# Performance work log

Hardware: AMD Instinct MI355X
Metric: run time of the kernel (lower is better)

Reference implementation:

```python
import jax, jax.numpy as jnp
import numpy as np

B, S, D, H = 2, 2048, 1024, 16
DH = D // H

def setup_inputs() -> dict:
    key = jax.random.key(0)
    ks = jax.random.split(key, 6)
    scale = 0.02
    return {
        "x":  jax.random.normal(ks[0], (B, S, D), jnp.float32),
        "Wq": jax.random.normal(ks[1], (D, D), jnp.float32) * scale,
        "Wk": jax.random.normal(ks[2], (D, D), jnp.float32) * scale,
        "Wv": jax.random.normal(ks[3], (D, D), jnp.float32) * scale,
        "Wo": jax.random.normal(ks[4], (D, D), jnp.float32) * scale,
        "bo": jnp.zeros((D,), jnp.float32),
    }

def reference(x, Wq, Wk, Wv, Wo, bo):
    b, s, d = x.shape
    h, dh = H, DH
    # projections -> [b, h, s, dh]
    def split_heads(t):
        return t.reshape(b, s, h, dh).transpose(0, 2, 1, 3)
    q = split_heads(x @ Wq)
    k = split_heads(x @ Wk)
    v = split_heads(x @ Wv)
    # scaled causal attention
    scores = jnp.einsum('bhqd,bhkd->bhqk', q, k) / jnp.sqrt(jnp.float32(dh))
    causal = jnp.tril(jnp.ones((s, s), bool))
    scores = jnp.where(causal[None, None], scores, -jnp.inf)
    attn = jax.nn.softmax(scores, axis=-1)
    # dropout p=0.0 -> identity
    ctx = jnp.einsum('bhqk,bhkd->bhqd', attn, v)
    ctx = ctx.transpose(0, 2, 1, 3).reshape(b, s, d)
    return ctx @ Wo + bo
```

## Files before the change

### kernel.cpp

```cpp
#include <hip/hip_runtime.h>


typedef _Float16 f16;
typedef _Float16 f16x8 __attribute__((ext_vector_type(8)));
typedef _Float16 f16x4 __attribute__((ext_vector_type(4)));
typedef float    f32x4 __attribute__((ext_vector_type(4)));

__device__ __forceinline__ void gload16(const void* g, void* l) {
  __builtin_amdgcn_global_load_lds(
      (const __attribute__((address_space(1))) void*)g,
      (__attribute__((address_space(3))) void*)l, 16, 0, 0);
}

__global__ void cvt_x(const float* __restrict__ x, f16* __restrict__ xb) {
  int idx = blockIdx.x * 256 + threadIdx.x;
  float4 v = ((const float4*)x)[idx];
  f16x4 o = { (f16)v.x, (f16)v.y, (f16)v.z, (f16)v.w };
  ((f16x4*)xb)[idx] = o;
}

__global__ void cvt_w(const float* __restrict__ W0, const float* __restrict__ W1,
                      const float* __restrict__ W2, const float* __restrict__ W3,
                      f16* __restrict__ T0, f16* __restrict__ T1,
                      f16* __restrict__ T2, f16* __restrict__ T3) {
  const float* W = blockIdx.z == 0 ? W0 : blockIdx.z == 1 ? W1 : blockIdx.z == 2 ? W2 : W3;
  f16*        Tt = blockIdx.z == 0 ? T0 : blockIdx.z == 1 ? T1 : blockIdx.z == 2 ? T2 : T3;
  __shared__ f16 tile[64][65];
  int tid = threadIdx.x;
  int k0 = blockIdx.y * 64, n0 = blockIdx.x * 64;
  int rr = tid >> 4, cc = (tid & 15) * 4;
#pragma unroll
  for (int p = 0; p < 4; ++p) {
    int r = rr + p * 16;
    float4 v = *(const float4*)(W + (size_t)(k0 + r) * 1024 + n0 + cc);
    tile[r][cc + 0] = (f16)v.x; tile[r][cc + 1] = (f16)v.y;
    tile[r][cc + 2] = (f16)v.z; tile[r][cc + 3] = (f16)v.w;
  }
  __syncthreads();
#pragma unroll
  for (int p = 0; p < 4; ++p) {
    int r = rr + p * 16;
    f16x4 v;
#pragma unroll
    for (int j = 0; j < 4; ++j) v[j] = tile[cc + j][r];
    *(f16x4*)(Tt + (size_t)(n0 + r) * 1024 + k0 + cc) = v;
  }
}

template <int MODE>
__global__ __launch_bounds__(256, 2)
void gemm_k(const f16* __restrict__ A, const f16* __restrict__ Bt,
            f16* __restrict__ oQ, f16* __restrict__ oK, f16* __restrict__ oV,
            float* __restrict__ oO, const float* __restrict__ bias) {
  constexpr int Kd = 1024;
  __shared__ f16 smem[2 * 128 * 64];
  f16* sA = smem;
  f16* sB = smem + 128 * 64;
  const int tid = threadIdx.x;
  const int lane = tid & 63, wid = tid >> 6;
  const int wr = wid >> 1, wc = wid & 1;
  const int bm = blockIdx.y * 128, bn = blockIdx.x * 128;

  f32x4 acc[4][4] = {};

  for (int k0 = 0; k0 < Kd; k0 += 64) {
#pragma unroll
    for (int p = 0; p < 4; ++p) {
      int c = p * 256 + tid;
      int row = c >> 3;
      int gc = (c & 7) ^ (row & 7);
      gload16(A + (size_t)(bm + row) * Kd + k0 + gc * 8, sA + c * 8);
      gload16(Bt + (size_t)(bn + row) * Kd + k0 + gc * 8, sB + c * 8);
    }
    __syncthreads();
#pragma unroll
    for (int ks = 0; ks < 2; ++ks) {
      f16x8 af[4], bf[4];
#pragma unroll
      for (int m = 0; m < 4; ++m) {
        int row = wr * 64 + m * 16 + (lane & 15);
        int j = (ks * 4 + (lane >> 4)) ^ (row & 7);
        af[m] = *(const f16x8*)((const char*)sA + row * 128 + j * 16);
      }
#pragma unroll
      for (int n = 0; n < 4; ++n) {
        int row = wc * 64 + n * 16 + (lane & 15);
        int j = (ks * 4 + (lane >> 4)) ^ (row & 7);
        bf[n] = *(const f16x8*)((const char*)sB + row * 128 + j * 16);
      }
#pragma unroll
      for (int m = 0; m < 4; ++m)
#pragma unroll
        for (int n = 0; n < 4; ++n)
          acc[m][n] = __builtin_amdgcn_mfma_f32_16x16x32_f16(af[m], bf[n], acc[m][n], 0, 0, 0);
    }
    __syncthreads();
  }

  if constexpr (MODE == 2) {
#pragma unroll
    for (int m = 0; m < 4; ++m) {
      int rbase = bm + wr * 64 + m * 16 + ((lane >> 4) << 2);
#pragma unroll
      for (int n = 0; n < 4; ++n) {
        int ncol = bn + wc * 64 + n * 16 + (lane & 15);
        float bv = bias[ncol];
#pragma unroll
        for (int i = 0; i < 4; ++i)
          oO[(size_t)(rbase + i) * 1024 + ncol] = acc[m][n][i] + bv;
      }
    }
  } else {
    const int seg = bn >> 10;
    if (seg < 2) {
      f16* dst = seg == 0 ? oQ : oK;
#pragma unroll
      for (int m = 0; m < 4; ++m) {
        int rbase = bm + wr * 64 + m * 16 + ((lane >> 4) << 2);
#pragma unroll
        for (int n = 0; n < 4; ++n) {
          int ncol = (bn & 1023) + wc * 64 + n * 16 + (lane & 15);
          int h = ncol >> 6, dh = ncol & 63;
#pragma unroll
          for (int i = 0; i < 4; ++i) {
            int rr = rbase + i;
            int b = rr >> 11, s = rr & 2047;
            dst[(((size_t)(b * 16 + h) * 2048 + s) << 6) + dh] = (f16)acc[m][n][i];
          }
        }
      }
    } else {
      f16* T64 = smem;
      int b = bm >> 11, sbase = bm & 2047;
      int bnl = bn & 1023;
#pragma unroll
      for (int p = 0; p < 2; ++p) {
        if (wr == p) {
#pragma unroll
          for (int m = 0; m < 4; ++m)
#pragma unroll
            for (int n = 0; n < 4; ++n)
#pragma unroll
              for (int i = 0; i < 4; ++i) {
                int rl = m * 16 + ((lane >> 4) << 2) + i;
                int col = wc * 64 + n * 16 + (lane & 15);
                T64[rl * 132 + col] = (f16)acc[m][n][i];
              }
        }
        __syncthreads();
#pragma unroll
        for (int it = 0; it < 4; ++it) {
          int oc = it * 256 + tid;
          int ocol = oc >> 3;
          int och = oc & 7;
          f16x8 v;
#pragma unroll
          for (int j = 0; j < 8; ++j) v[j] = T64[(och * 8 + j) * 132 + ocol];
          int ncol = bnl + ocol;
          int h = ncol >> 6, dh = ncol & 63;
          *(f16x8*)(oV + ((size_t)((b * 16 + h) * 64 + dh) << 11) + sbase + p * 64 + och * 8) = v;
        }
        __syncthreads();
      }
    }
  }
}

__global__ __launch_bounds__(256, 2)
void attn_k(const f16* __restrict__ Q, const f16* __restrict__ Kg,
            const f16* __restrict__ Vt, f16* __restrict__ ctx) {
  __shared__ f16 sK[64 * 64];
  __shared__ f16 sV[64 * 64];
  __shared__ f16 sP[4][16 * 64];
  const int tid = threadIdx.x, lane = tid & 63, wid = tid >> 6;
  const int bh = blockIdx.y;
  const int b = bh >> 4, h = bh & 15;
  const f16* Qb = Q + ((size_t)bh << 17);
  const f16* Kb = Kg + ((size_t)bh << 17);
  const f16* Vb = Vt + ((size_t)bh << 17);
  const float SC = 0.1803368801f;

  for (int half = 0; half < 2; ++half) {
    const int qt = half == 0 ? blockIdx.x : 31 - blockIdx.x;
    const int qbase = qt * 64 + wid * 16;
    const int qg = qbase + (lane & 15);
    const int qmax_w = qbase + 15;

    const int qrow_a = qbase + (lane & 15);
    f16x8 qf[2];
    qf[0] = *(const f16x8*)(Qb + (size_t)qrow_a * 64 + ((lane >> 4) << 3));
    qf[1] = *(const f16x8*)(Qb + (size_t)qrow_a * 64 + 32 + ((lane >> 4) << 3));

    f32x4 acc[4] = {};
    float m_run = -INFINITY, l_run = 0.f;

    for (int kt = 0; kt <= qt; ++kt) {
#pragma unroll
      for (int p = 0; p < 2; ++p) {
        int c = p * 256 + tid;
        int row = c >> 3;
        int gc = (c & 7) ^ (row & 7);
        gload16(Kb + (size_t)(kt * 64 + row) * 64 + gc * 8, sK + c * 8);
        gload16(Vb + (size_t)row * 2048 + kt * 64 + gc * 8, sV + c * 8);
      }
      __syncthreads();

      f32x4 sf[4];
#pragma unroll
      for (int kc = 0; kc < 4; ++kc) {
        if (kt * 64 + kc * 16 <= qmax_w) {
          f32x4 z = {};
#pragma unroll
          for (int ks = 0; ks < 2; ++ks) {
            int row = kc * 16 + (lane & 15);
            int j = (ks * 4 + (lane >> 4)) ^ (row & 7);
            f16x8 kf = *(const f16x8*)((const char*)sK + row * 128 + j * 16);
            z = __builtin_amdgcn_mfma_f32_16x16x32_f16(kf, qf[ks], z, 0, 0, 0);
          }
          sf[kc] = z;
        } else {
          sf[kc] = (f32x4){-1e30f, -1e30f, -1e30f, -1e30f};
        }
      }
#pragma unroll
      for (int kc = 0; kc < 4; ++kc) {
        if (kt * 64 + kc * 16 + 15 > qbase) {
#pragma unroll
          for (int i = 0; i < 4; ++i) {
            int kg = kt * 64 + kc * 16 + ((lane >> 4) << 2) + i;
            sf[kc][i] = (kg <= qg) ? sf[kc][i] * SC : -1e30f;
          }
        } else {
#pragma unroll
          for (int i = 0; i < 4; ++i) sf[kc][i] *= SC;
        }
      }
      float v01 = fmaxf(fmaxf(sf[0][0], sf[0][1]), fmaxf(sf[0][2], sf[0][3]));
      float v23 = fmaxf(fmaxf(sf[1][0], sf[1][1]), fmaxf(sf[1][2], sf[1][3]));
      float v45 = fmaxf(fmaxf(sf[2][0], sf[2][1]), fmaxf(sf[2][2], sf[2][3]));
      float v67 = fmaxf(fmaxf(sf[3][0], sf[3][1]), fmaxf(sf[3][2], sf[3][3]));
      float v = fmaxf(fmaxf(v01, v23), fmaxf(v45, v67));
      v = fmaxf(v, __shfl_xor(v, 16));
      v = fmaxf(v, __shfl_xor(v, 32));
      float mn = fmaxf(m_run, v);
      float scl = __builtin_amdgcn_exp2f(m_run - mn);
      m_run = mn;
      float ls = 0.f;
#pragma unroll
      for (int kc = 0; kc < 4; ++kc)
#pragma unroll
        for (int i = 0; i < 4; ++i) {
          float p = __builtin_amdgcn_exp2f(sf[kc][i] - mn);
          sf[kc][i] = p;
          ls += p;
        }
      ls += __shfl_xor(ls, 16);
      ls += __shfl_xor(ls, 32);
      l_run = l_run * scl + ls;
#pragma unroll
      for (int i = 0; i < 4; ++i) {
        float sb = __shfl(scl, ((lane >> 4) << 2) + i);
#pragma unroll
        for (int d = 0; d < 4; ++d) acc[d][i] *= sb;
      }
      char* Pw = (char*)(sP[wid]);
#pragma unroll
      for (int kc = 0; kc < 4; ++kc) {
        int kbase = kc * 16 + ((lane >> 4) << 2);
        int ch = kbase >> 3;
        f16x4 pv = { (f16)sf[kc][0], (f16)sf[kc][1], (f16)sf[kc][2], (f16)sf[kc][3] };
        *(f16x4*)(Pw + (lane & 15) * 128 + ((ch ^ (lane & 7)) << 4) + ((kbase & 7) << 1)) = pv;
      }
#pragma unroll
      for (int kk = 0; kk < 2; ++kk) {
        if (kt * 64 + kk * 32 <= qmax_w) {
          int prow = lane & 15;
          int pj = (kk * 4 + (lane >> 4)) ^ (prow & 7);
          f16x8 pa = *(const f16x8*)(Pw + prow * 128 + pj * 16);
#pragma unroll
          for (int d = 0; d < 4; ++d) {
            int vrow = d * 16 + (lane & 15);
            int vj = (kk * 4 + (lane >> 4)) ^ (vrow & 7);
            f16x8 vf = *(const f16x8*)((const char*)sV + vrow * 128 + vj * 16);
            acc[d] = __builtin_amdgcn_mfma_f32_16x16x32_f16(pa, vf, acc[d], 0, 0, 0);
          }
        }
      }
      __syncthreads();
    }
#pragma unroll
    for (int i = 0; i < 4; ++i) {
      float lb = __shfl(l_run, ((lane >> 4) << 2) + i);
      float r = 1.f / lb;
      int s = qbase + ((lane >> 4) << 2) + i;
#pragma unroll
      for (int d = 0; d < 4; ++d) {
        float val = acc[d][i] * r;
        ctx[((size_t)(b * 2048 + s) << 10) + (h << 6) + (d << 4) + (lane & 15)] = (f16)val;
      }
    }
  }
}

extern "C" void kernel_launch(void* const* d_in, const int* in_sizes, int n_in,
                              void* d_out, int out_size, void* d_ws, size_t ws_size,
                              hipStream_t stream) {
  const float* x  = (const float*)d_in[0];
  const float* Wq = (const float*)d_in[1];
  const float* Wk = (const float*)d_in[2];
  const float* Wv = (const float*)d_in[3];
  const float* Wo = (const float*)d_in[4];
  const float* bo = (const float*)d_in[5];
  char* ws = (char*)d_ws;
  f16* xb   = (f16*)(ws);
  f16* Wcat = (f16*)(ws + ((size_t)8  << 20));
  f16* Wot  = (f16*)(ws + ((size_t)14 << 20));
  f16* Qb   = (f16*)(ws + ((size_t)16 << 20));
  f16* Kb   = (f16*)(ws + ((size_t)24 << 20));
  f16* Vtb  = (f16*)(ws + ((size_t)32 << 20));
  f16* ctx  = (f16*)(ws + ((size_t)40 << 20));
  const size_t MM = (size_t)1024 * 1024;

  hipLaunchKernelGGL(cvt_x, dim3(4096), dim3(256), 0, stream, x, xb);
  hipLaunchKernelGGL(cvt_w, dim3(16, 16, 4), dim3(256), 0, stream,
                     Wq, Wk, Wv, Wo, Wcat, Wcat + MM, Wcat + 2 * MM, Wot);
  hipLaunchKernelGGL((gemm_k<0>), dim3(24, 32), dim3(256), 0, stream,
                     xb, Wcat, Qb, Kb, Vtb, nullptr, nullptr);
  hipLaunchKernelGGL(attn_k, dim3(16, 32), dim3(256), 0, stream, Qb, Kb, Vtb, ctx);
  hipLaunchKernelGGL((gemm_k<2>), dim3(8, 32), dim3(256), 0, stream,
                     ctx, Wot, nullptr, nullptr, nullptr, (float*)d_out, bo);
}
```

Measured before the change: 201.6 us.

## Fuse x fp32-to-fp16 conversion into QKV GEMM and split-K output projection

```diff
diff --git a/kernel.cpp b/kernel.cpp
--- a/kernel.cpp
+++ b/kernel.cpp
@@ -10,13 +10,6 @@
   __builtin_amdgcn_global_load_lds(
       (const __attribute__((address_space(1))) void*)g,
       (__attribute__((address_space(3))) void*)l, 16, 0, 0);
-}
-
-__global__ void cvt_x(const float* __restrict__ x, f16* __restrict__ xb) {
-  int idx = blockIdx.x * 256 + threadIdx.x;
-  float4 v = ((const float4*)x)[idx];
-  f16x4 o = { (f16)v.x, (f16)v.y, (f16)v.z, (f16)v.w };
-  ((f16x4*)xb)[idx] = o;
 }
 
 __global__ void cvt_w(const float* __restrict__ W0, const float* __restrict__ W1,
@@ -49,7 +42,8 @@
 
 template <int MODE>
 __global__ __launch_bounds__(256, 2)
-void gemm_k(const f16* __restrict__ A, const f16* __restrict__ Bt,
+void gemm_k(const float* __restrict__ Af32, const f16* __restrict__ Af16,
+            const f16* __restrict__ Bt,
             f16* __restrict__ oQ, f16* __restrict__ oK, f16* __restrict__ oV,
             float* __restrict__ oO, const float* __restrict__ bias) {
   constexpr int Kd = 1024;
@@ -60,16 +54,27 @@
   const int lane = tid & 63, wid = tid >> 6;
   const int wr = wid >> 1, wc = wid & 1;
   const int bm = blockIdx.y * 128, bn = blockIdx.x * 128;
+  const int kbeg = (MODE == 3) ? blockIdx.z * 512 : 0;
+  const int kend = (MODE == 3) ? kbeg + 512 : Kd;
 
   f32x4 acc[4][4] = {};
 
-  for (int k0 = 0; k0 < Kd; k0 += 64) {
+  for (int k0 = kbeg; k0 < kend; k0 += 64) {
 #pragma unroll
     for (int p = 0; p < 4; ++p) {
       int c = p * 256 + tid;
       int row = c >> 3;
       int gc = (c & 7) ^ (row & 7);
-      gload16(A + (size_t)(bm + row) * Kd + k0 + gc * 8, sA + c * 8);
+      if constexpr (MODE == 0) {
+        const float* src = Af32 + (size_t)(bm + row) * Kd + k0 + gc * 8;
+        float4 u0 = *(const float4*)(src);
+        float4 u1 = *(const float4*)(src + 4);
+        f16x8 w = { (f16)u0.x, (f16)u0.y, (f16)u0.z, (f16)u0.w,
+                    (f16)u1.x, (f16)u1.y, (f16)u1.z, (f16)u1.w };
+        *(f16x8*)(sA + c * 8) = w;
+      } else {
+        gload16(Af16 + (size_t)(bm + row) * Kd + k0 + gc * 8, sA + c * 8);
+      }
       gload16(Bt + (size_t)(bn + row) * Kd + k0 + gc * 8, sB + c * 8);
     }
     __syncthreads();
@@ -97,17 +102,18 @@
     __syncthreads();
   }
 
-  if constexpr (MODE == 2) {
+  if constexpr (MODE == 3) {
+    const bool addb = (blockIdx.z == 0);
 #pragma unroll
     for (int m = 0; m < 4; ++m) {
       int rbase = bm + wr * 64 + m * 16 + ((lane >> 4) << 2);
 #pragma unroll
       for (int n = 0; n < 4; ++n) {
         int ncol = bn + wc * 64 + n * 16 + (lane & 15);
-        float bv = bias[ncol];
+        float bv = addb ? bias[ncol] : 0.f;
 #pragma unroll
         for (int i = 0; i < 4; ++i)
-          oO[(size_t)(rbase + i) * 1024 + ncol] = acc[m][n][i] + bv;
+          atomicAdd(&oO[(size_t)(rbase + i) * 1024 + ncol], acc[m][n][i] + bv);
       }
     }
   } else {
@@ -312,7 +318,6 @@
   const float* Wo = (const float*)d_in[4];
   const float* bo = (const float*)d_in[5];
   char* ws = (char*)d_ws;
-  f16* xb   = (f16*)(ws);
   f16* Wcat = (f16*)(ws + ((size_t)8  << 20));
   f16* Wot  = (f16*)(ws + ((size_t)14 << 20));
   f16* Qb   = (f16*)(ws + ((size_t)16 << 20));
@@ -321,12 +326,12 @@
   f16* ctx  = (f16*)(ws + ((size_t)40 << 20));
   const size_t MM = (size_t)1024 * 1024;
 
-  hipLaunchKernelGGL(cvt_x, dim3(4096), dim3(256), 0, stream, x, xb);
+  hipMemsetAsync(d_out, 0, (size_t)out_size * sizeof(float), stream);
   hipLaunchKernelGGL(cvt_w, dim3(16, 16, 4), dim3(256), 0, stream,
                      Wq, Wk, Wv, Wo, Wcat, Wcat + MM, Wcat + 2 * MM, Wot);
   hipLaunchKernelGGL((gemm_k<0>), dim3(24, 32), dim3(256), 0, stream,
-                     xb, Wcat, Qb, Kb, Vtb, nullptr, nullptr);
+                     x, nullptr, Wcat, Qb, Kb, Vtb, nullptr, nullptr);
   hipLaunchKernelGGL(attn_k, dim3(16, 32), dim3(256), 0, stream, Qb, Kb, Vtb, ctx);
-  hipLaunchKernelGGL((gemm_k<2>), dim3(8, 32), dim3(256), 0, stream,
-                     ctx, Wot, nullptr, nullptr, nullptr, (float*)d_out, bo);
-}
+  hipLaunchKernelGGL((gemm_k<3>), dim3(8, 32, 2), dim3(256), 0, stream,
+                     nullptr, ctx, Wot, nullptr, nullptr, nullptr, (float*)d_out, bo);
+}
```

Result: slower. 226.2 us (+12.2%).

## Split attention q-tile pairs into separate blocks and narrow output GEMM tile

Applied to the files above, without the earlier changes.

```diff
diff --git a/kernel.cpp b/kernel.cpp
--- a/kernel.cpp
+++ b/kernel.cpp
@@ -53,15 +53,17 @@
             f16* __restrict__ oQ, f16* __restrict__ oK, f16* __restrict__ oV,
             float* __restrict__ oO, const float* __restrict__ bias) {
   constexpr int Kd = 1024;
-  __shared__ f16 smem[2 * 128 * 64];
+  constexpr int BN = (MODE == 2) ? 64 : 128;
+  constexpr int NF = BN / 32;
+  __shared__ f16 smem[128 * 64 + BN * 64];
   f16* sA = smem;
   f16* sB = smem + 128 * 64;
   const int tid = threadIdx.x;
   const int lane = tid & 63, wid = tid >> 6;
   const int wr = wid >> 1, wc = wid & 1;
-  const int bm = blockIdx.y * 128, bn = blockIdx.x * 128;
-
-  f32x4 acc[4][4] = {};
+  const int bm = blockIdx.y * 128, bn = blockIdx.x * BN;
+
+  f32x4 acc[4][NF] = {};
 
   for (int k0 = 0; k0 < Kd; k0 += 64) {
 #pragma unroll
@@ -70,12 +72,18 @@
       int row = c >> 3;
       int gc = (c & 7) ^ (row & 7);
       gload16(A + (size_t)(bm + row) * Kd + k0 + gc * 8, sA + c * 8);
+    }
+#pragma unroll
+    for (int p = 0; p < NF; ++p) {
+      int c = p * 256 + tid;
+      int row = c >> 3;
+      int gc = (c & 7) ^ (row & 7);
       gload16(Bt + (size_t)(bn + row) * Kd + k0 + gc * 8, sB + c * 8);
     }
     __syncthreads();
 #pragma unroll
     for (int ks = 0; ks < 2; ++ks) {
-      f16x8 af[4], bf[4];
+      f16x8 af[4], bf[NF];
 #pragma unroll
       for (int m = 0; m < 4; ++m) {
         int row = wr * 64 + m * 16 + (lane & 15);
@@ -83,15 +91,15 @@
         af[m] = *(const f16x8*)((const char*)sA + row * 128 + j * 16);
       }
 #pragma unroll
-      for (int n = 0; n < 4; ++n) {
-        int row = wc * 64 + n * 16 + (lane & 15);
+      for (int n = 0; n < NF; ++n) {
+        int row = wc * (BN / 2) + n * 16 + (lane & 15);
         int j = (ks * 4 + (lane >> 4)) ^ (row & 7);
         bf[n] = *(const f16x8*)((const char*)sB + row * 128 + j * 16);
       }
 #pragma unroll
       for (int m = 0; m < 4; ++m)
 #pragma unroll
-        for (int n = 0; n < 4; ++n)
+        for (int n = 0; n < NF; ++n)
           acc[m][n] = __builtin_amdgcn_mfma_f32_16x16x32_f16(af[m], bf[n], acc[m][n], 0, 0, 0);
     }
     __syncthreads();
@@ -102,8 +110,8 @@
     for (int m = 0; m < 4; ++m) {
       int rbase = bm + wr * 64 + m * 16 + ((lane >> 4) << 2);
 #pragma unroll
-      for (int n = 0; n < 4; ++n) {
-        int ncol = bn + wc * 64 + n * 16 + (lane & 15);
+      for (int n = 0; n < NF; ++n) {
+        int ncol = bn + wc * (BN / 2) + n * 16 + (lane & 15);
         float bv = bias[ncol];
 #pragma unroll
         for (int i = 0; i < 4; ++i)
@@ -118,7 +126,7 @@
       for (int m = 0; m < 4; ++m) {
         int rbase = bm + wr * 64 + m * 16 + ((lane >> 4) << 2);
 #pragma unroll
-        for (int n = 0; n < 4; ++n) {
+        for (int n = 0; n < NF; ++n) {
           int ncol = (bn & 1023) + wc * 64 + n * 16 + (lane & 15);
           int h = ncol >> 6, dh = ncol & 63;
 #pragma unroll
@@ -139,7 +147,7 @@
 #pragma unroll
           for (int m = 0; m < 4; ++m)
 #pragma unroll
-            for (int n = 0; n < 4; ++n)
+            for (int n = 0; n < NF; ++n)
 #pragma unroll
               for (int i = 0; i < 4; ++i) {
                 int rl = m * 16 + ((lane >> 4) << 2) + i;
@@ -175,129 +183,127 @@
   const int tid = threadIdx.x, lane = tid & 63, wid = tid >> 6;
   const int bh = blockIdx.y;
   const int b = bh >> 4, h = bh & 15;
+  const int qt = ((bh >> 3) & 1) ? (31 - (int)blockIdx.x) : (int)blockIdx.x;
   const f16* Qb = Q + ((size_t)bh << 17);
   const f16* Kb = Kg + ((size_t)bh << 17);
   const f16* Vb = Vt + ((size_t)bh << 17);
   const float SC = 0.1803368801f;
 
-  for (int half = 0; half < 2; ++half) {
-    const int qt = half == 0 ? blockIdx.x : 31 - blockIdx.x;
-    const int qbase = qt * 64 + wid * 16;
-    const int qg = qbase + (lane & 15);
-    const int qmax_w = qbase + 15;
-
-    const int qrow_a = qbase + (lane & 15);
-    f16x8 qf[2];
-    qf[0] = *(const f16x8*)(Qb + (size_t)qrow_a * 64 + ((lane >> 4) << 3));
-    qf[1] = *(const f16x8*)(Qb + (size_t)qrow_a * 64 + 32 + ((lane >> 4) << 3));
-
-    f32x4 acc[4] = {};
-    float m_run = -INFINITY, l_run = 0.f;
-
-    for (int kt = 0; kt <= qt; ++kt) {
-#pragma unroll
-      for (int p = 0; p < 2; ++p) {
-        int c = p * 256 + tid;
-        int row = c >> 3;
-        int gc = (c & 7) ^ (row & 7);
-        gload16(Kb + (size_t)(kt * 64 + row) * 64 + gc * 8, sK + c * 8);
-        gload16(Vb + (size_t)row * 2048 + kt * 64 + gc * 8, sV + c * 8);
-      }
-      __syncthreads();
-
-      f32x4 sf[4];
-#pragma unroll
-      for (int kc = 0; kc < 4; ++kc) {
-        if (kt * 64 + kc * 16 <= qmax_w) {
-          f32x4 z = {};
-#pragma unroll
-          for (int ks = 0; ks < 2; ++ks) {
-            int row = kc * 16 + (lane & 15);
-            int j = (ks * 4 + (lane >> 4)) ^ (row & 7);
-            f16x8 kf = *(const f16x8*)((const char*)sK + row * 128 + j * 16);
-            z = __builtin_amdgcn_mfma_f32_16x16x32_f16(kf, qf[ks], z, 0, 0, 0);
-          }
-          sf[kc] = z;
-        } else {
-          sf[kc] = (f32x4){-1e30f, -1e30f, -1e30f, -1e30f};
-        }
-      }
-#pragma unroll
-      for (int kc = 0; kc < 4; ++kc) {
-        if (kt * 64 + kc * 16 + 15 > qbase) {
-#pragma unroll
-          for (int i = 0; i < 4; ++i) {
-            int kg = kt * 64 + kc * 16 + ((lane >> 4) << 2) + i;
-            sf[kc][i] = (kg <= qg) ? sf[kc][i] * SC : -1e30f;
-          }
-        } else {
-#pragma unroll
-          for (int i = 0; i < 4; ++i) sf[kc][i] *= SC;
-        }
-      }
-      float v01 = fmaxf(fmaxf(sf[0][0], sf[0][1]), fmaxf(sf[0][2], sf[0][3]));
-      float v23 = fmaxf(fmaxf(sf[1][0], sf[1][1]), fmaxf(sf[1][2], sf[1][3]));
-      float v45 = fmaxf(fmaxf(sf[2][0], sf[2][1]), fmaxf(sf[2][2], sf[2][3]));
-      float v67 = fmaxf(fmaxf(sf[3][0], sf[3][1]), fmaxf(sf[3][2], sf[3][3]));
-      float v = fmaxf(fmaxf(v01, v23), fmaxf(v45, v67));
-      v = fmaxf(v, __shfl_xor(v, 16));
-      v = fmaxf(v, __shfl_xor(v, 32));
-      float mn = fmaxf(m_run, v);
-      float scl = __builtin_amdgcn_exp2f(m_run - mn);
-      m_run = mn;
-      float ls = 0.f;
-#pragma unroll
-      for (int kc = 0; kc < 4; ++kc)
+  const int qbase = qt * 64 + wid * 16;
+  const int qg = qbase + (lane & 15);
+  const int qmax_w = qbase + 15;
+
+  const int qrow_a = qbase + (lane & 15);
+  f16x8 qf[2];
+  qf[0] = *(const f16x8*)(Qb + (size_t)qrow_a * 64 + ((lane >> 4) << 3));
+  qf[1] = *(const f16x8*)(Qb + (size_t)qrow_a * 64 + 32 + ((lane >> 4) << 3));
+
+  f32x4 acc[4] = {};
+  float m_run = -INFINITY, l_run = 0.f;
+
+  for (int kt = 0; kt <= qt; ++kt) {
+#pragma unroll
+    for (int p = 0; p < 2; ++p) {
+      int c = p * 256 + tid;
+      int row = c >> 3;
+      int gc = (c & 7) ^ (row & 7);
+      gload16(Kb + (size_t)(kt * 64 + row) * 64 + gc * 8, sK + c * 8);
+      gload16(Vb + (size_t)row * 2048 + kt * 64 + gc * 8, sV + c * 8);
+    }
+    __syncthreads();
+
+    f32x4 sf[4];
+#pragma unroll
+    for (int kc = 0; kc < 4; ++kc) {
+      if (kt * 64 + kc * 16 <= qmax_w) {
+        f32x4 z = {};
+#pragma unroll
+        for (int ks = 0; ks < 2; ++ks) {
+          int row = kc * 16 + (lane & 15);
+          int j = (ks * 4 + (lane >> 4)) ^ (row & 7);
+          f16x8 kf = *(const f16x8*)((const char*)sK + row * 128 + j * 16);
+          z = __builtin_amdgcn_mfma_f32_16x16x32_f16(kf, qf[ks], z, 0, 0, 0);
+        }
+        sf[kc] = z;
+      } else {
+        sf[kc] = (f32x4){-1e30f, -1e30f, -1e30f, -1e30f};
+      }
+    }
+#pragma unroll
+    for (int kc = 0; kc < 4; ++kc) {
+      if (kt * 64 + kc * 16 + 15 > qbase) {
 #pragma unroll
         for (int i = 0; i < 4; ++i) {
-          float p = __builtin_amdgcn_exp2f(sf[kc][i] - mn);
-          sf[kc][i] = p;
-          ls += p;
-        }
-      ls += __shfl_xor(ls, 16);
-      ls += __shfl_xor(ls, 32);
-      l_run = l_run * scl + ls;
+          int kg = kt * 64 + kc * 16 + ((lane >> 4) << 2) + i;
+          sf[kc][i] = (kg <= qg) ? sf[kc][i] * SC : -1e30f;
+        }
+      } else {
+#pragma unroll
+        for (int i = 0; i < 4; ++i) sf[kc][i] *= SC;
+      }
+    }
+    float v01 = fmaxf(fmaxf(sf[0][0], sf[0][1]), fmaxf(sf[0][2], sf[0][3]));
+    float v23 = fmaxf(fmaxf(sf[1][0], sf[1][1]), fmaxf(sf[1][2], sf[1][3]));
+    float v45 = fmaxf(fmaxf(sf[2][0], sf[2][1]), fmaxf(sf[2][2], sf[2][3]));
+    float v67 = fmaxf(fmaxf(sf[3][0], sf[3][1]), fmaxf(sf[3][2], sf[3][3]));
+    float v = fmaxf(fmaxf(v01, v23), fmaxf(v45, v67));
+    v = fmaxf(v, __shfl_xor(v, 16));
+    v = fmaxf(v, __shfl_xor(v, 32));
+    float mn = fmaxf(m_run, v);
+    float scl = __builtin_amdgcn_exp2f(m_run - mn);
+    m_run = mn;
+    float ls = 0.f;
+#pragma unroll
+    for (int kc = 0; kc < 4; ++kc)
 #pragma unroll
       for (int i = 0; i < 4; ++i) {
-        float sb = __shfl(scl, ((lane >> 4) << 2) + i);
-#pragma unroll
-        for (int d = 0; d < 4; ++d) acc[d][i] *= sb;
-      }
-      char* Pw = (char*)(sP[wid]);
-#pragma unroll
-      for (int kc = 0; kc < 4; ++kc) {
-        int kbase = kc * 16 + ((lane >> 4) << 2);
-        int ch = kbase >> 3;
-        f16x4 pv = { (f16)sf[kc][0], (f16)sf[kc][1], (f16)sf[kc][2], (f16)sf[kc][3] };
-        *(f16x4*)(Pw + (lane & 15) * 128 + ((ch ^ (lane & 7)) << 4) + ((kbase & 7) << 1)) = pv;
-      }
-#pragma unroll
-      for (int kk = 0; kk < 2; ++kk) {
-        if (kt * 64 + kk * 32 <= qmax_w) {
-          int prow = lane & 15;
-          int pj = (kk * 4 + (lane >> 4)) ^ (prow & 7);
-          f16x8 pa = *(const f16x8*)(Pw + prow * 128 + pj * 16);
-#pragma unroll
-          for (int d = 0; d < 4; ++d) {
-            int vrow = d * 16 + (lane & 15);
-            int vj = (kk * 4 + (lane >> 4)) ^ (vrow & 7);
-            f16x8 vf = *(const f16x8*)((const char*)sV + vrow * 128 + vj * 16);
-            acc[d] = __builtin_amdgcn_mfma_f32_16x16x32_f16(pa, vf, acc[d], 0, 0, 0);
-          }
-        }
-      }
-      __syncthreads();
-    }
+        float p = __builtin_amdgcn_exp2f(sf[kc][i] - mn);
+        sf[kc][i] = p;
+        ls += p;
+      }
+    ls += __shfl_xor(ls, 16);
+    ls += __shfl_xor(ls, 32);
+    l_run = l_run * scl + ls;
 #pragma unroll
     for (int i = 0; i < 4; ++i) {
-      float lb = __shfl(l_run, ((lane >> 4) << 2) + i);
-      float r = 1.f / lb;
-      int s = qbase + ((lane >> 4) << 2) + i;
-#pragma unroll
-      for (int d = 0; d < 4; ++d) {
-        float val = acc[d][i] * r;
-        ctx[((size_t)(b * 2048 + s) << 10) + (h << 6) + (d << 4) + (lane & 15)] = (f16)val;
-      }
+      float sb = __shfl(scl, ((lane >> 4) << 2) + i);
+#pragma unroll
+      for (int d = 0; d < 4; ++d) acc[d][i] *= sb;
+    }
+    char* Pw = (char*)(sP[wid]);
+#pragma unroll
+    for (int kc = 0; kc < 4; ++kc) {
+      int kbase = kc * 16 + ((lane >> 4) << 2);
+      int ch = kbase >> 3;
+      f16x4 pv = { (f16)sf[kc][0], (f16)sf[kc][1], (f16)sf[kc][2], (f16)sf[kc][3] };
+      *(f16x4*)(Pw + (lane & 15) * 128 + ((ch ^ (lane & 7)) << 4) + ((kbase & 7) << 1)) = pv;
+    }
+#pragma unroll
+    for (int kk = 0; kk < 2; ++kk) {
+      if (kt * 64 + kk * 32 <= qmax_w) {
+        int prow = lane & 15;
+        int pj = (kk * 4 + (lane >> 4)) ^ (prow & 7);
+        f16x8 pa = *(const f16x8*)(Pw + prow * 128 + pj * 16);
+#pragma unroll
+        for (int d = 0; d < 4; ++d) {
+          int vrow = d * 16 + (lane & 15);
+          int vj = (kk * 4 + (lane >> 4)) ^ (vrow & 7);
+          f16x8 vf = *(const f16x8*)((const char*)sV + vrow * 128 + vj * 16);
+          acc[d] = __builtin_amdgcn_mfma_f32_16x16x32_f16(pa, vf, acc[d], 0, 0, 0);
+        }
+      }
+    }
+    __syncthreads();
+  }
+#pragma unroll
+  for (int i = 0; i < 4; ++i) {
+    float lb = __shfl(l_run, ((lane >> 4) << 2) + i);
+    float r = 1.f / lb;
+    int s = qbase + ((lane >> 4) << 2) + i;
+#pragma unroll
+    for (int d = 0; d < 4; ++d) {
+      float val = acc[d][i] * r;
+      ctx[((size_t)(b * 2048 + s) << 10) + (h << 6) + (d << 4) + (lane & 15)] = (f16)val;
     }
   }
 }
@@ -326,7 +332,7 @@
                      Wq, Wk, Wv, Wo, Wcat, Wcat + MM, Wcat + 2 * MM, Wot);
   hipLaunchKernelGGL((gemm_k<0>), dim3(24, 32), dim3(256), 0, stream,
                      xb, Wcat, Qb, Kb, Vtb, nullptr, nullptr);
-  hipLaunchKernelGGL(attn_k, dim3(16, 32), dim3(256), 0, stream, Qb, Kb, Vtb, ctx);
-  hipLaunchKernelGGL((gemm_k<2>), dim3(8, 32), dim3(256), 0, stream,
+  hipLaunchKernelGGL(attn_k, dim3(32, 32), dim3(256), 0, stream, Qb, Kb, Vtb, ctx);
+  hipLaunchKernelGGL((gemm_k<2>), dim3(16, 32), dim3(256), 0, stream,
                      ctx, Wot, nullptr, nullptr, nullptr, (float*)d_out, bo);
 }
```

Result: faster. 188.2 us (-6.7%).
